# Performance work log

Hardware: AMD Instinct MI355X
Metric: run time of the kernel (lower is better)

The kernel has to match this reference:

```python
import jax, jax.numpy as jnp
import numpy as np

INPUT_DIM = 100
LATENT_DIM = 128
HIDDEN_DIM = 64
BATCH = 16384


def setup_inputs() -> dict:
    key = jax.random.key(0)
    ku, k1, kb1, k2, kb2 = jax.random.split(key, 5)
    u = jax.random.normal(ku, (BATCH, INPUT_DIM), dtype=jnp.float32)
    # PyTorch Linear init: U(-1/sqrt(fan_in), 1/sqrt(fan_in))
    s1 = 1.0 / np.sqrt(INPUT_DIM)
    s2 = 1.0 / np.sqrt(HIDDEN_DIM)
    W1 = jax.random.uniform(k1, (LATENT_DIM, HIDDEN_DIM, INPUT_DIM), jnp.float32, -s1, s1)
    b1 = jax.random.uniform(kb1, (LATENT_DIM, HIDDEN_DIM), jnp.float32, -s1, s1)
    W2 = jax.random.uniform(k2, (LATENT_DIM, HIDDEN_DIM), jnp.float32, -s2, s2)  # out_features=1 squeezed
    b2 = jax.random.uniform(kb2, (LATENT_DIM,), jnp.float32, -s2, s2)
    return {"u": u, "W1": W1, "b1": b1, "W2": W2, "b2": b2}


def reference(u, W1, b1, W2, b2):
    # All latent_dim branches batched as one grouped GEMM.
    # h: [batch, latent, hidden]
    h = jnp.tanh(jnp.einsum('bi,khi->bkh', u, W1) + b1[None, :, :])
    # out: [batch, latent]  (second Linear has output dim 1, squeezed)
    out = jnp.einsum('bkh,kh->bk', h, W2) + b2[None, :]
    return out
```

## Files before the change

### kernel.cpp

```cpp
#include <hip/hip_runtime.h>

#define BATCH 16384
#define LATENT 128
#define HIDDEN 64
#define INDIM 100
#define KPAD 128

typedef short shortx8 __attribute__((ext_vector_type(8)));
typedef float floatx4 __attribute__((ext_vector_type(4)));

__device__ __forceinline__ short f2bf(float f) {
    union { float f; unsigned u; } v; v.f = f;
    unsigned r = v.u + 0x7FFF + ((v.u >> 16) & 1);
    return (short)(r >> 16);
}

#if __has_builtin(__builtin_amdgcn_exp2f)
#define EXP2F(x) __builtin_amdgcn_exp2f(x)
#else
#define EXP2F(x) __exp2f(x)
#endif
#if __has_builtin(__builtin_amdgcn_rcpf)
#define RCPF(x) __builtin_amdgcn_rcpf(x)
#else
#define RCPF(x) (1.0f / (x))
#endif

#define N_U_CHUNKS (BATCH * KPAD / 8)
#define N_W_CHUNKS (LATENT * HIDDEN * KPAD / 8)

__global__ __launch_bounds__(256) void prep_all(const float* __restrict__ u,
                                                const float* __restrict__ W1,
                                                const float* __restrict__ b1,
                                                shortx8* __restrict__ uf,
                                                shortx8* __restrict__ wf) {
    int c = blockIdx.x * 256 + threadIdx.x;
    if (c < N_U_CHUNKS) {
        int lane = c & 63;
        int kt = (c >> 6) & 3;
        int g = c >> 8;
        int row = g * 16 + (lane & 15);
        int kbase = kt * 32 + ((lane >> 4) << 3);
        shortx8 v;
        if (kbase + 7 < INDIM) {
            const float4* p = (const float4*)(u + row * INDIM + kbase);
            float4 f0 = p[0], f1 = p[1];
            v[0] = f2bf(f0.x); v[1] = f2bf(f0.y); v[2] = f2bf(f0.z); v[3] = f2bf(f0.w);
            v[4] = f2bf(f1.x); v[5] = f2bf(f1.y); v[6] = f2bf(f1.z); v[7] = f2bf(f1.w);
        } else {
#pragma unroll
            for (int j = 0; j < 8; j++) {
                int k = kbase + j;
                float f = (k < INDIM) ? u[row * INDIM + k] : (k == INDIM ? 1.0f : 0.0f);
                v[j] = f2bf(f);
            }
        }
        uf[c] = v;
    } else {
        int c2 = c - N_U_CHUNKS;
        int lane = c2 & 63;
        int kt = (c2 >> 6) & 3;
        int nt = (c2 >> 8) & 3;
        int lat = c2 >> 10;
        int h = nt * 16 + (lane & 15);
        int hw = lat * HIDDEN + h;
        int kbase = kt * 32 + ((lane >> 4) << 3);
        shortx8 v;
        if (kbase + 7 < INDIM) {
            const float4* p = (const float4*)(W1 + hw * INDIM + kbase);
            float4 f0 = p[0], f1 = p[1];
            v[0] = f2bf(f0.x); v[1] = f2bf(f0.y); v[2] = f2bf(f0.z); v[3] = f2bf(f0.w);
            v[4] = f2bf(f1.x); v[5] = f2bf(f1.y); v[6] = f2bf(f1.z); v[7] = f2bf(f1.w);
        } else {
#pragma unroll
            for (int j = 0; j < 8; j++) {
                int k = kbase + j;
                float f = (k < INDIM) ? W1[hw * INDIM + k] : (k == INDIM ? b1[hw] : 0.0f);
                v[j] = f2bf(f);
            }
        }
        wf[c2] = v;
    }
}

__global__ __launch_bounds__(256, 4) void branch_mlp(const shortx8* __restrict__ uf,
                                                     const shortx8* __restrict__ wf,
                                                     const float* __restrict__ W2,
                                                     const float* __restrict__ b2,
                                                     float* __restrict__ out) {
    int tid = threadIdx.x;
    int lane = tid & 63;
    int w = tid >> 6;
    int bx = blockIdx.x;
    int by = blockIdx.y;
    int g0 = bx * 8 + w * 2;
    int q = lane >> 4;

    shortx8 ub[2][4];
    const shortx8* ua = uf + (size_t)g0 * 4 * 64 + lane;
#pragma unroll
    for (int gi = 0; gi < 2; gi++)
#pragma unroll
        for (int kt = 0; kt < 4; kt++)
            ub[gi][kt] = ua[(gi * 4 + kt) * 64];

#pragma unroll
    for (int li = 0; li < 4; li++) {
        int lat = by * 4 + li;
        const shortx8* wb = wf + (size_t)lat * 16 * 64 + lane;

        float4 w2v[4];
#pragma unroll
        for (int nt = 0; nt < 4; nt++)
            w2v[nt] = *(const float4*)(W2 + lat * HIDDEN + nt * 16 + q * 4);
        float b2v = b2[lat];

        shortx8 afr[4][4];
#pragma unroll
        for (int nt = 0; nt < 4; nt++)
#pragma unroll
            for (int kt = 0; kt < 4; kt++)
                afr[nt][kt] = wb[(nt * 4 + kt) * 64];

        floatx4 acc[2][4] = {};
#pragma unroll
        for (int kt = 0; kt < 4; kt++)
#pragma unroll
            for (int nt = 0; nt < 4; nt++)
#pragma unroll
                for (int gi = 0; gi < 2; gi++)
                    acc[gi][nt] = __builtin_amdgcn_mfma_f32_16x16x32_bf16(afr[nt][kt], ub[gi][kt], acc[gi][nt], 0, 0, 0);

#pragma unroll
        for (int gi = 0; gi < 2; gi++) {
            float s = 0.0f;
#pragma unroll
            for (int nt = 0; nt < 4; nt++)
#pragma unroll
                for (int r = 0; r < 4; r++) {
                    float x = acc[gi][nt][r];
                    float e = EXP2F(x * 2.88539008177793f);
                    float rr = RCPF(e + 1.0f);
                    float t = fmaf(-2.0f, rr, 1.0f);
                    s = fmaf(t, w2v[nt][r], s);
                }
            s += __shfl_xor(s, 16, 64);
            s += __shfl_xor(s, 32, 64);
            if (lane < 16)
                out[((g0 + gi) * 16 + lane) * LATENT + lat] = s + b2v;
        }
    }
}

__global__ __launch_bounds__(256) void fallback_kernel(const float* __restrict__ u, const float* __restrict__ W1,
                                                       const float* __restrict__ b1, const float* __restrict__ W2,
                                                       const float* __restrict__ b2, float* __restrict__ out) {
    int idx = blockIdx.x * 256 + threadIdx.x;
    if (idx >= BATCH * LATENT) return;
    int b = idx >> 7;
    int lat = idx & 127;
    const float* ub = u + b * INDIM;
    float s = 0.0f;
    for (int h = 0; h < HIDDEN; h++) {
        const float* wp = W1 + (lat * HIDDEN + h) * INDIM;
        float dd = b1[lat * HIDDEN + h];
        for (int k = 0; k < INDIM; k++) dd += ub[k] * wp[k];
        s += tanhf(dd) * W2[lat * HIDDEN + h];
    }
    out[idx] = s + b2[lat];
}

extern "C" void kernel_launch(void* const* d_in, const int* in_sizes, int n_in,
                              void* d_out, int out_size, void* d_ws, size_t ws_size,
                              hipStream_t stream) {
    const float* u  = (const float*)d_in[0];
    const float* W1 = (const float*)d_in[1];
    const float* b1 = (const float*)d_in[2];
    const float* W2 = (const float*)d_in[3];
    const float* b2 = (const float*)d_in[4];
    float* out = (float*)d_out;

    const size_t UF_BYTES = (size_t)BATCH * KPAD * 2;
    const size_t WF_BYTES = (size_t)LATENT * HIDDEN * KPAD * 2;

    if (ws_size < UF_BYTES + WF_BYTES) {
        fallback_kernel<<<(BATCH * LATENT + 255) / 256, 256, 0, stream>>>(u, W1, b1, W2, b2, out);
        return;
    }

    shortx8* uf = (shortx8*)d_ws;
    shortx8* wf = (shortx8*)((char*)d_ws + UF_BYTES);

    prep_all<<<(N_U_CHUNKS + N_W_CHUNKS) / 256, 256, 0, stream>>>(u, W1, b1, uf, wf);
    branch_mlp<<<dim3(BATCH / 128, LATENT / 4), 256, 0, stream>>>(uf, wf, W2, b2, out);
}
```

Before: 124.7 us.

## Fold tanh scale into weights and restructure branch kernel per latent

The tanh scale factor is folded into W1 and b1 during the bf16 conversion. The -2 and +1 terms of tanh are folded into W2 and a precomputed effective b2, which removes a multiply and an FMA per hidden element. The main kernel now gives each block a single latent and loops over 8 batch groups per wave, keeping the weight fragments in registers. Each wave reloads u fragments per group. Per-block latent weight loads go from 4 latents to 1, but u is now streamed 128 times overall instead of 32, and bf16 rounding of the scaled weights changes numerics slightly.

```diff
diff --git a/kernel.cpp b/kernel.cpp
--- a/kernel.cpp
+++ b/kernel.cpp
@@ -5,6 +5,7 @@
 #define HIDDEN 64
 #define INDIM 100
 #define KPAD 128
+#define TANH_SCALE 2.885390081777927f
 
 typedef short shortx8 __attribute__((ext_vector_type(8)));
 typedef float floatx4 __attribute__((ext_vector_type(4)));
@@ -32,8 +33,11 @@
 __global__ __launch_bounds__(256) void prep_all(const float* __restrict__ u,
                                                 const float* __restrict__ W1,
                                                 const float* __restrict__ b1,
+                                                const float* __restrict__ W2,
+                                                const float* __restrict__ b2,
                                                 shortx8* __restrict__ uf,
-                                                shortx8* __restrict__ wf) {
+                                                shortx8* __restrict__ wf,
+                                                float* __restrict__ b2eff) {
     int c = blockIdx.x * 256 + threadIdx.x;
     if (c < N_U_CHUNKS) {
         int lane = c & 63;
@@ -56,7 +60,7 @@
             }
         }
         uf[c] = v;
-    } else {
+    } else if (c < N_U_CHUNKS + N_W_CHUNKS) {
         int c2 = c - N_U_CHUNKS;
         int lane = c2 & 63;
         int kt = (c2 >> 6) & 3;
@@ -69,86 +73,91 @@
         if (kbase + 7 < INDIM) {
             const float4* p = (const float4*)(W1 + hw * INDIM + kbase);
             float4 f0 = p[0], f1 = p[1];
-            v[0] = f2bf(f0.x); v[1] = f2bf(f0.y); v[2] = f2bf(f0.z); v[3] = f2bf(f0.w);
-            v[4] = f2bf(f1.x); v[5] = f2bf(f1.y); v[6] = f2bf(f1.z); v[7] = f2bf(f1.w);
+            v[0] = f2bf(f0.x * TANH_SCALE); v[1] = f2bf(f0.y * TANH_SCALE);
+            v[2] = f2bf(f0.z * TANH_SCALE); v[3] = f2bf(f0.w * TANH_SCALE);
+            v[4] = f2bf(f1.x * TANH_SCALE); v[5] = f2bf(f1.y * TANH_SCALE);
+            v[6] = f2bf(f1.z * TANH_SCALE); v[7] = f2bf(f1.w * TANH_SCALE);
         } else {
 #pragma unroll
             for (int j = 0; j < 8; j++) {
                 int k = kbase + j;
-                float f = (k < INDIM) ? W1[hw * INDIM + k] : (k == INDIM ? b1[hw] : 0.0f);
+                float f = (k < INDIM) ? W1[hw * INDIM + k] * TANH_SCALE
+                                      : (k == INDIM ? b1[hw] * TANH_SCALE : 0.0f);
                 v[j] = f2bf(f);
             }
         }
         wf[c2] = v;
+    } else {
+        int lat = c - (N_U_CHUNKS + N_W_CHUNKS);
+        if (lat < LATENT) {
+            float s = b2[lat];
+            const float* wp = W2 + lat * HIDDEN;
+#pragma unroll 8
+            for (int h = 0; h < HIDDEN; h++) s += wp[h];
+            b2eff[lat] = s;
+        }
     }
 }
 
 __global__ __launch_bounds__(256, 4) void branch_mlp(const shortx8* __restrict__ uf,
                                                      const shortx8* __restrict__ wf,
                                                      const float* __restrict__ W2,
-                                                     const float* __restrict__ b2,
+                                                     const float* __restrict__ b2eff,
                                                      float* __restrict__ out) {
     int tid = threadIdx.x;
     int lane = tid & 63;
     int w = tid >> 6;
     int bx = blockIdx.x;
-    int by = blockIdx.y;
-    int g0 = bx * 8 + w * 2;
+    int lat = bx >> 5;
+    int G0 = (bx & 31) * 32 + w * 8;
     int q = lane >> 4;
 
-    shortx8 ub[2][4];
-    const shortx8* ua = uf + (size_t)g0 * 4 * 64 + lane;
-#pragma unroll
-    for (int gi = 0; gi < 2; gi++)
+    shortx8 afr[4][4];
+    const shortx8* wb = wf + (size_t)lat * 16 * 64 + lane;
+#pragma unroll
+    for (int nt = 0; nt < 4; nt++)
 #pragma unroll
         for (int kt = 0; kt < 4; kt++)
-            ub[gi][kt] = ua[(gi * 4 + kt) * 64];
-
-#pragma unroll
-    for (int li = 0; li < 4; li++) {
-        int lat = by * 4 + li;
-        const shortx8* wb = wf + (size_t)lat * 16 * 64 + lane;
-
-        float4 w2v[4];
+            afr[nt][kt] = wb[(nt * 4 + kt) * 64];
+
+    float4 w2v[4];
+#pragma unroll
+    for (int nt = 0; nt < 4; nt++) {
+        float4 t = *(const float4*)(W2 + lat * HIDDEN + nt * 16 + q * 4);
+        w2v[nt] = make_float4(-2.0f * t.x, -2.0f * t.y, -2.0f * t.z, -2.0f * t.w);
+    }
+    float b2v = b2eff[lat];
+
+    const shortx8* ua = uf + (size_t)G0 * 4 * 64 + lane;
+    float* outp = out + (size_t)G0 * 16 * LATENT + lat;
+
+#pragma unroll
+    for (int g = 0; g < 8; g++) {
+        shortx8 ub[4];
+#pragma unroll
+        for (int kt = 0; kt < 4; kt++)
+            ub[kt] = ua[(g * 4 + kt) * 64];
+
+        floatx4 acc[4] = {};
+#pragma unroll
+        for (int kt = 0; kt < 4; kt++)
+#pragma unroll
+            for (int nt = 0; nt < 4; nt++)
+                acc[nt] = __builtin_amdgcn_mfma_f32_16x16x32_bf16(afr[nt][kt], ub[kt], acc[nt], 0, 0, 0);
+
+        float s = 0.0f;
 #pragma unroll
         for (int nt = 0; nt < 4; nt++)
-            w2v[nt] = *(const float4*)(W2 + lat * HIDDEN + nt * 16 + q * 4);
-        float b2v = b2[lat];
-
-        shortx8 afr[4][4];
-#pragma unroll
-        for (int nt = 0; nt < 4; nt++)
-#pragma unroll
-            for (int kt = 0; kt < 4; kt++)
-                afr[nt][kt] = wb[(nt * 4 + kt) * 64];
-
-        floatx4 acc[2][4] = {};
-#pragma unroll
-        for (int kt = 0; kt < 4; kt++)
-#pragma unroll
-            for (int nt = 0; nt < 4; nt++)
-#pragma unroll
-                for (int gi = 0; gi < 2; gi++)
-                    acc[gi][nt] = __builtin_amdgcn_mfma_f32_16x16x32_bf16(afr[nt][kt], ub[gi][kt], acc[gi][nt], 0, 0, 0);
-
-#pragma unroll
-        for (int gi = 0; gi < 2; gi++) {
-            float s = 0.0f;
-#pragma unroll
-            for (int nt = 0; nt < 4; nt++)
-#pragma unroll
-                for (int r = 0; r < 4; r++) {
-                    float x = acc[gi][nt][r];
-                    float e = EXP2F(x * 2.88539008177793f);
-                    float rr = RCPF(e + 1.0f);
-                    float t = fmaf(-2.0f, rr, 1.0f);
-                    s = fmaf(t, w2v[nt][r], s);
-                }
-            s += __shfl_xor(s, 16, 64);
-            s += __shfl_xor(s, 32, 64);
-            if (lane < 16)
-                out[((g0 + gi) * 16 + lane) * LATENT + lat] = s + b2v;
-        }
+#pragma unroll
+            for (int r = 0; r < 4; r++) {
+                float e = EXP2F(acc[nt][r]);
+                float rr = RCPF(e + 1.0f);
+                s = fmaf((&w2v[nt].x)[r], rr, s);
+            }
+        s += __shfl_xor(s, 16, 64);
+        s += __shfl_xor(s, 32, 64);
+        if (lane < 16)
+            outp[(g * 16 + lane) * LATENT] = s + b2v;
     }
 }
 
@@ -182,15 +191,17 @@
 
     const size_t UF_BYTES = (size_t)BATCH * KPAD * 2;
     const size_t WF_BYTES = (size_t)LATENT * HIDDEN * KPAD * 2;
-
-    if (ws_size < UF_BYTES + WF_BYTES) {
+    const size_t B2_BYTES = LATENT * sizeof(float);
+
+    if (ws_size < UF_BYTES + WF_BYTES + B2_BYTES) {
         fallback_kernel<<<(BATCH * LATENT + 255) / 256, 256, 0, stream>>>(u, W1, b1, W2, b2, out);
         return;
     }
 
     shortx8* uf = (shortx8*)d_ws;
     shortx8* wf = (shortx8*)((char*)d_ws + UF_BYTES);
-
-    prep_all<<<(N_U_CHUNKS + N_W_CHUNKS) / 256, 256, 0, stream>>>(u, W1, b1, uf, wf);
-    branch_mlp<<<dim3(BATCH / 128, LATENT / 4), 256, 0, stream>>>(uf, wf, W2, b2, out);
-}
+    float* b2eff = (float*)((char*)d_ws + UF_BYTES + WF_BYTES);
+
+    prep_all<<<(N_U_CHUNKS + N_W_CHUNKS) / 256 + 1, 256, 0, stream>>>(u, W1, b1, W2, b2, uf, wf, b2eff);
+    branch_mlp<<<4096, 256, 0, stream>>>(uf, wf, W2, b2eff, out);
+}
```

After: 112.8 us. 1.11x faster.
